# Kernel tuning notes

Hardware: AMD Instinct MI355X
Metric: run time of the kernel (lower is better)

## Reference

```python
import jax, jax.numpy as jnp
import numpy as np

TEMPERATURE = 10.0
NUM_PROBES = 100


def setup_inputs() -> dict:
    key = jax.random.key(0)
    k1, k2 = jax.random.split(key)
    N, C = 50000, 20
    y_pred = jax.random.normal(k1, (N, C), dtype=jnp.float32)
    s = jax.random.randint(k2, (N,), 0, 2, dtype=jnp.int32)
    return {"y_pred": y_pred, "s": s}


def reference(y_pred, s):
    # y_pred: [N, C], s: [N] in {0,1}
    # Per-class probing grid: 100 points from min to max of that class's preds.
    # torch's .item() detaches min/max from the graph -> stop_gradient here.
    mn = jax.lax.stop_gradient(jnp.min(y_pred, axis=0))  # [C]
    mx = jax.lax.stop_gradient(jnp.max(y_pred, axis=0))  # [C]
    frac = jnp.arange(NUM_PROBES, dtype=y_pred.dtype) / (NUM_PROBES - 1)  # [P]
    grid = mn[:, None] + (mx - mn)[:, None] * frac[None, :]  # [C, P]

    # Smoothed ECDF via sigmoid: diff has shape [C, P, N]
    preds = y_pred.T  # [C, N]
    sig = jax.nn.sigmoid(TEMPERATURE * (grid[:, :, None] - preds[:, None, :]))

    mask0 = (s == 0).astype(y_pred.dtype)  # [N]
    mask1 = (s == 1).astype(y_pred.dtype)
    n0 = jnp.sum(mask0)
    n1 = jnp.sum(mask1)

    # Masked group means == per-group mean since sigmoid is elementwise
    cdf0 = jnp.einsum('cpn,n->cp', sig, mask0) / n0  # [C, P]
    cdf1 = jnp.einsum('cpn,n->cp', sig, mask1) / n1  # [C, P]

    delta = jnp.abs(cdf0 - cdf1)  # [C, P]
    # loss_i = max over probes; final = max over classes -> global max
    return jnp.max(delta)
```

## Files before the change

kernel.cpp:

```cpp
#include <hip/hip_runtime.h>

#define NC 20
#define NP 100
#define PG 10
#define NPG (NP / PG)
#define SLICES 10
#define TPB 256
#define KLOG2E 14.426950408889634f
#define NBS 256

__device__ __forceinline__ float fexp2(float x) {
#if __has_builtin(__builtin_amdgcn_exp2f)
    return __builtin_amdgcn_exp2f(x);
#else
    return __builtin_exp2f(x);
#endif
}
__device__ __forceinline__ float sgpr_f(float x) {
    return __uint_as_float(__builtin_amdgcn_readfirstlane(__float_as_uint(x)));
}

template<bool WRITE_T>
__global__ __launch_bounds__(256)
void prep_kernel(const float* __restrict__ y, const int* __restrict__ s,
                 float* __restrict__ E, float* __restrict__ sf,
                 float* __restrict__ part_mn, float* __restrict__ part_mx,
                 int* __restrict__ part_cnt, int N, int ncap) {
    const int q = blockIdx.y;
    const int bx = blockIdx.x;
    float mn[4] = {3.4e38f, 3.4e38f, 3.4e38f, 3.4e38f};
    float mx[4] = {-3.4e38f, -3.4e38f, -3.4e38f, -3.4e38f};
    int cnt = 0;
    const int stride = gridDim.x * 256;
    for (int n = bx * 256 + threadIdx.x; n < ncap; n += stride) {
        if (n < N) {
            float4 f = ((const float4*)y)[n * 5 + q];
            float v[4] = {f.x, f.y, f.z, f.w};
#pragma unroll
            for (int cc = 0; cc < 4; ++cc) {
                mn[cc] = fminf(mn[cc], v[cc]);
                mx[cc] = fmaxf(mx[cc], v[cc]);
                if (WRITE_T) E[(size_t)(4 * q + cc) * ncap + n] = fexp2(v[cc] * KLOG2E);
            }
            if (q == 0) {
                int m = s[n];
                cnt += m;
                if (WRITE_T) sf[n] = (float)m;
            }
        } else if (WRITE_T) {
#pragma unroll
            for (int cc = 0; cc < 4; ++cc)
                E[(size_t)(4 * q + cc) * ncap + n] = __builtin_inff();
            if (q == 0) sf[n] = 0.f;
        }
    }
#pragma unroll
    for (int off = 1; off < 64; off <<= 1) {
#pragma unroll
        for (int cc = 0; cc < 4; ++cc) {
            mn[cc] = fminf(mn[cc], __shfl_xor(mn[cc], off));
            mx[cc] = fmaxf(mx[cc], __shfl_xor(mx[cc], off));
        }
        cnt += __shfl_xor(cnt, off);
    }
    __shared__ float smn[4][4], smx[4][4];
    __shared__ int scnt[4];
    const int wave = threadIdx.x >> 6, lane = threadIdx.x & 63;
    if (lane == 0) {
#pragma unroll
        for (int cc = 0; cc < 4; ++cc) { smn[wave][cc] = mn[cc]; smx[wave][cc] = mx[cc]; }
        scnt[wave] = cnt;
    }
    __syncthreads();
    const int t = threadIdx.x;
    if (t < 4) {
        part_mn[(4 * q + t) * NBS + bx] =
            fminf(fminf(smn[0][t], smn[1][t]), fminf(smn[2][t], smn[3][t]));
    } else if (t < 8) {
        int cc = t - 4;
        part_mx[(4 * q + cc) * NBS + bx] =
            fmaxf(fmaxf(smx[0][cc], smx[1][cc]), fmaxf(smx[2][cc], smx[3][cc]));
    } else if (t == 8 && q == 0) {
        part_cnt[bx] = scnt[0] + scnt[1] + scnt[2] + scnt[3];
    }
}

template<bool RAW>
__global__ __launch_bounds__(256)
void cdf2_kernel(const float* __restrict__ E, const float* __restrict__ sf,
                 const float* __restrict__ y, const int* __restrict__ s,
                 const float* __restrict__ part_mn, const float* __restrict__ part_mx,
                 const int* __restrict__ part_cnt,
                 float* __restrict__ acc_part, int N, int ncap, int nb) {
    const int c = blockIdx.x;
    const int pg = blockIdx.y;
    float lmn = 3.4e38f, lmx = -3.4e38f;
    int lcnt = 0;
    for (int t = threadIdx.x; t < nb; t += 256) {
        lmn = fminf(lmn, part_mn[c * NBS + t]);
        lmx = fmaxf(lmx, part_mx[c * NBS + t]);
        lcnt += part_cnt[t];
    }
#pragma unroll
    for (int off = 1; off < 64; off <<= 1) {
        lmn = fminf(lmn, __shfl_xor(lmn, off));
        lmx = fmaxf(lmx, __shfl_xor(lmx, off));
        lcnt += __shfl_xor(lcnt, off);
    }
    __shared__ float rmn[4], rmx[4];
    __shared__ int rcnt[4];
    const int wave = threadIdx.x >> 6, lane = threadIdx.x & 63;
    if (lane == 0) { rmn[wave] = lmn; rmx[wave] = lmx; rcnt[wave] = lcnt; }
    __syncthreads();
    const float mn = fminf(fminf(rmn[0], rmn[1]), fminf(rmn[2], rmn[3]));
    const float mx = fmaxf(fmaxf(rmx[0], rmx[1]), fmaxf(rmx[2], rmx[3]));
    const int n1 = rcnt[0] + rcnt[1] + rcnt[2] + rcnt[3];
    const float inv1 = 1.0f / (float)n1;
    const float inv0 = 1.0f / (float)(N - n1);
    const float sA = sgpr_f(inv1 + inv0);
    const float sB = sgpr_f(-inv0);

    int p = pg * PG + (lane % PG);
    float frac = (float)p / 99.0f;
    float g = fmaf(mx - mn, frac, mn);
    float Gl = fexp2(-g * KLOG2E);
    float G[PG];
#pragma unroll
    for (int j = 0; j < PG; ++j) G[j] = sgpr_f(__shfl(Gl, j));

    float d[PG];
#pragma unroll
    for (int j = 0; j < PG; ++j) d[j] = 0.f;

    const int nq = ncap >> 2;
    if (!RAW) {
        const float4* E4 = (const float4*)(E + (size_t)c * ncap);
        const float4* S4 = (const float4*)sf;
#pragma unroll 2
        for (int q = blockIdx.z * TPB + threadIdx.x; q < nq; q += TPB * SLICES) {
            float4 ev = E4[q];
            float4 mv = S4[q];
            float ee[4] = {ev.x, ev.y, ev.z, ev.w};
            float ww[4];
            ww[0] = fmaf(mv.x, sA, sB); ww[1] = fmaf(mv.y, sA, sB);
            ww[2] = fmaf(mv.z, sA, sB); ww[3] = fmaf(mv.w, sA, sB);
#pragma unroll
            for (int e = 0; e < 4; ++e) {
#pragma unroll
                for (int j = 0; j < PG; ++j) {
                    float t = fmaf(ee[e], G[j], 1.0f);
                    float r = __builtin_amdgcn_rcpf(t);
                    d[j] = fmaf(r, ww[e], d[j]);
                }
            }
        }
    } else {
        for (int q = blockIdx.z * TPB + threadIdx.x; q < nq; q += TPB * SLICES) {
#pragma unroll
            for (int e = 0; e < 4; ++e) {
                int n = q * 4 + e;
                bool valid = n < N;
                float ev = valid ? fexp2(y[(size_t)n * NC + c] * KLOG2E)
                                 : __builtin_inff();
                float w  = valid ? fmaf((float)s[n], sA, sB) : 0.f;
#pragma unroll
                for (int j = 0; j < PG; ++j) {
                    float t = fmaf(ev, G[j], 1.0f);
                    float r = __builtin_amdgcn_rcpf(t);
                    d[j] = fmaf(r, w, d[j]);
                }
            }
        }
    }
#pragma unroll
    for (int off = 1; off < 64; off <<= 1) {
#pragma unroll
        for (int j = 0; j < PG; ++j) d[j] += __shfl_xor(d[j], off);
    }
    __shared__ float sd[4][PG];
    if (lane == 0) {
#pragma unroll
        for (int j = 0; j < PG; ++j) sd[wave][j] = d[j];
    }
    __syncthreads();
    if (threadIdx.x < PG) {
        int j = threadIdx.x;
        float v = (sd[0][j] + sd[1][j]) + (sd[2][j] + sd[3][j]);
        acc_part[(size_t)(c * NP + pg * PG + j) * SLICES + blockIdx.z] = v;
    }
}

__global__ __launch_bounds__(256)
void finalize_kernel(const float* __restrict__ acc_part, float* __restrict__ out) {
    float m = 0.f;
    for (int i = threadIdx.x; i < NC * NP; i += 256) {
        const float* base = acc_part + (size_t)i * SLICES;
        float sum = 0.f;
#pragma unroll
        for (int z = 0; z < SLICES; ++z) sum += base[z];
        m = fmaxf(m, fabsf(sum));
    }
#pragma unroll
    for (int off = 1; off < 64; off <<= 1)
        m = fmaxf(m, __shfl_xor(m, off));
    __shared__ float red[4];
    const int wave = threadIdx.x >> 6, lane = threadIdx.x & 63;
    if (lane == 0) red[wave] = m;
    __syncthreads();
    if (threadIdx.x == 0)
        out[0] = fmaxf(fmaxf(red[0], red[1]), fmaxf(red[2], red[3]));
}

extern "C" void kernel_launch(void* const* d_in, const int* in_sizes, int n_in,
                              void* d_out, int out_size, void* d_ws, size_t ws_size,
                              hipStream_t stream) {
    const float* y = (const float*)d_in[0];
    const int* s   = (const int*)d_in[1];
    const int N = in_sizes[1];
    const int ncap = ((N + 1023) / 1024) * 1024;
    int nb = ncap / 256;
    if (nb > NBS) nb = NBS;

    unsigned char* ws = (unsigned char*)d_ws;
    float* part_mn  = (float*)ws;
    float* part_mx  = (float*)(ws + 20480);
    int*   part_cnt = (int*)  (ws + 40960);
    float* acc_part = (float*)(ws + 45056);
    float* E        = (float*)(ws + 131072);
    float* sf       = (float*)(ws + 131072 + (size_t)4 * NC * ncap);
    size_t need = 131072 + (size_t)4 * (NC + 1) * ncap;
    bool fat = ws_size >= need;

    dim3 gA(nb, 5);
    if (fat) prep_kernel<true ><<<gA, 256, 0, stream>>>(y, s, E, sf, part_mn, part_mx, part_cnt, N, ncap);
    else     prep_kernel<false><<<gA, 256, 0, stream>>>(y, s, nullptr, nullptr, part_mn, part_mx, part_cnt, N, ncap);

    dim3 gB(NC, NPG, SLICES);
    if (fat) cdf2_kernel<false><<<gB, 256, 0, stream>>>(E, sf, y, s, part_mn, part_mx, part_cnt, acc_part, N, ncap, nb);
    else     cdf2_kernel<true ><<<gB, 256, 0, stream>>>(nullptr, nullptr, y, s, part_mn, part_mx, part_cnt, acc_part, N, ncap, nb);

    finalize_kernel<<<1, 256, 0, stream>>>(acc_part, (float*)d_out);
}
```

Measured before the change: 33.15 us.

## Pack group mask into exp sign bit and fuse finalize via last-block atomics

The prep kernel now encodes the group label in the sign bit of each stored exp value instead of writing a separate float mask array. The CDF kernel recovers the weight from the sign and uses the absolute value for the sigmoid term, which removes one global load stream per element. The separate finalize launch is replaced by a per-(class, probe-group) atomic counter: the last slice block sums the partial results and does an atomicMax on the output. This saves a kernel launch and workspace traffic, but it relies on relaxed atomics for ordering and never zeroes the output before the atomicMax.

```diff
diff --git a/kernel.cpp b/kernel.cpp
--- a/kernel.cpp
+++ b/kernel.cpp
@@ -23,11 +23,14 @@
 template<bool WRITE_T>
 __global__ __launch_bounds__(256)
 void prep_kernel(const float* __restrict__ y, const int* __restrict__ s,
-                 float* __restrict__ E, float* __restrict__ sf,
+                 float* __restrict__ E,
                  float* __restrict__ part_mn, float* __restrict__ part_mx,
-                 int* __restrict__ part_cnt, int N, int ncap) {
+                 int* __restrict__ part_cnt, unsigned* __restrict__ cnt200,
+                 int N, int ncap) {
     const int q = blockIdx.y;
     const int bx = blockIdx.x;
+    if (q == 2 && bx == 0 && threadIdx.x < NC * NPG) cnt200[threadIdx.x] = 0u;
+
     float mn[4] = {3.4e38f, 3.4e38f, 3.4e38f, 3.4e38f};
     float mx[4] = {-3.4e38f, -3.4e38f, -3.4e38f, -3.4e38f};
     int cnt = 0;
@@ -36,22 +39,25 @@
         if (n < N) {
             float4 f = ((const float4*)y)[n * 5 + q];
             float v[4] = {f.x, f.y, f.z, f.w};
+            int m = 0;
+            if (q == 0) { m = s[n]; cnt += m; }
+            unsigned sgn = 0u;
+            if (WRITE_T && q == 0) sgn = m ? 0x80000000u : 0u;
+            if (WRITE_T) sgn = (s[n] ? 0x80000000u : 0u);
 #pragma unroll
             for (int cc = 0; cc < 4; ++cc) {
                 mn[cc] = fminf(mn[cc], v[cc]);
                 mx[cc] = fmaxf(mx[cc], v[cc]);
-                if (WRITE_T) E[(size_t)(4 * q + cc) * ncap + n] = fexp2(v[cc] * KLOG2E);
-            }
-            if (q == 0) {
-                int m = s[n];
-                cnt += m;
-                if (WRITE_T) sf[n] = (float)m;
+                if (WRITE_T) {
+                    float e = fexp2(v[cc] * KLOG2E);
+                    E[(size_t)(4 * q + cc) * ncap + n] =
+                        __uint_as_float(__float_as_uint(e) | sgn);
+                }
             }
         } else if (WRITE_T) {
 #pragma unroll
             for (int cc = 0; cc < 4; ++cc)
                 E[(size_t)(4 * q + cc) * ncap + n] = __builtin_inff();
-            if (q == 0) sf[n] = 0.f;
         }
     }
 #pragma unroll
@@ -87,11 +93,12 @@
 
 template<bool RAW>
 __global__ __launch_bounds__(256)
-void cdf2_kernel(const float* __restrict__ E, const float* __restrict__ sf,
+void cdf2_kernel(const float* __restrict__ E,
                  const float* __restrict__ y, const int* __restrict__ s,
                  const float* __restrict__ part_mn, const float* __restrict__ part_mx,
                  const int* __restrict__ part_cnt,
-                 float* __restrict__ acc_part, int N, int ncap, int nb) {
+                 float* __restrict__ acc_part, unsigned* __restrict__ cnt200,
+                 float* __restrict__ out, int N, int ncap, int nb) {
     const int c = blockIdx.x;
     const int pg = blockIdx.y;
     float lmn = 3.4e38f, lmx = -3.4e38f;
@@ -117,8 +124,9 @@
     const int n1 = rcnt[0] + rcnt[1] + rcnt[2] + rcnt[3];
     const float inv1 = 1.0f / (float)n1;
     const float inv0 = 1.0f / (float)(N - n1);
-    const float sA = sgpr_f(inv1 + inv0);
-    const float sB = sgpr_f(-inv0);
+    const float sAB = sgpr_f(inv1);
+    const float sB  = sgpr_f(-inv0);
+    const float sA1 = sgpr_f(inv1);
 
     int p = pg * PG + (lane % PG);
     float frac = (float)p / 99.0f;
@@ -135,20 +143,19 @@
     const int nq = ncap >> 2;
     if (!RAW) {
         const float4* E4 = (const float4*)(E + (size_t)c * ncap);
-        const float4* S4 = (const float4*)sf;
 #pragma unroll 2
         for (int q = blockIdx.z * TPB + threadIdx.x; q < nq; q += TPB * SLICES) {
             float4 ev = E4[q];
-            float4 mv = S4[q];
             float ee[4] = {ev.x, ev.y, ev.z, ev.w};
             float ww[4];
-            ww[0] = fmaf(mv.x, sA, sB); ww[1] = fmaf(mv.y, sA, sB);
-            ww[2] = fmaf(mv.z, sA, sB); ww[3] = fmaf(mv.w, sA, sB);
+#pragma unroll
+            for (int e = 0; e < 4; ++e)
+                ww[e] = (__float_as_int(ee[e]) < 0) ? sA1 : sB;
 #pragma unroll
             for (int e = 0; e < 4; ++e) {
 #pragma unroll
                 for (int j = 0; j < PG; ++j) {
-                    float t = fmaf(ee[e], G[j], 1.0f);
+                    float t = fmaf(fabsf(ee[e]), G[j], 1.0f);
                     float r = __builtin_amdgcn_rcpf(t);
                     d[j] = fmaf(r, ww[e], d[j]);
                 }
@@ -162,7 +169,7 @@
                 bool valid = n < N;
                 float ev = valid ? fexp2(y[(size_t)n * NC + c] * KLOG2E)
                                  : __builtin_inff();
-                float w  = valid ? fmaf((float)s[n], sA, sB) : 0.f;
+                float w  = valid ? ((s[n] != 0) ? sA1 : sB) : 0.f;
 #pragma unroll
                 for (int j = 0; j < PG; ++j) {
                     float t = fmaf(ev, G[j], 1.0f);
@@ -183,32 +190,42 @@
         for (int j = 0; j < PG; ++j) sd[wave][j] = d[j];
     }
     __syncthreads();
+    float* slot_base = acc_part + (size_t)(c * NP + pg * PG) * SLICES;
     if (threadIdx.x < PG) {
         int j = threadIdx.x;
         float v = (sd[0][j] + sd[1][j]) + (sd[2][j] + sd[3][j]);
-        acc_part[(size_t)(c * NP + pg * PG + j) * SLICES + blockIdx.z] = v;
-    }
-}
-
-__global__ __launch_bounds__(256)
-void finalize_kernel(const float* __restrict__ acc_part, float* __restrict__ out) {
-    float m = 0.f;
-    for (int i = threadIdx.x; i < NC * NP; i += 256) {
-        const float* base = acc_part + (size_t)i * SLICES;
-        float sum = 0.f;
-#pragma unroll
-        for (int z = 0; z < SLICES; ++z) sum += base[z];
-        m = fmaxf(m, fabsf(sum));
-    }
-#pragma unroll
-    for (int off = 1; off < 64; off <<= 1)
-        m = fmaxf(m, __shfl_xor(m, off));
-    __shared__ float red[4];
-    const int wave = threadIdx.x >> 6, lane = threadIdx.x & 63;
-    if (lane == 0) red[wave] = m;
-    __syncthreads();
-    if (threadIdx.x == 0)
-        out[0] = fmaxf(fmaxf(red[0], red[1]), fmaxf(red[2], red[3]));
+        __hip_atomic_store(slot_base + j * SLICES + blockIdx.z, v,
+                           __ATOMIC_RELAXED, __HIP_MEMORY_SCOPE_AGENT);
+    }
+    asm volatile("s_waitcnt vmcnt(0)" ::: "memory");
+    __shared__ int is_last;
+    if (threadIdx.x == 0) {
+        unsigned prev = __hip_atomic_fetch_add(&cnt200[c * NPG + pg], 1u,
+                                               __ATOMIC_RELAXED,
+                                               __HIP_MEMORY_SCOPE_AGENT);
+        is_last = (prev == SLICES - 1);
+    }
+    __syncthreads();
+    if (!is_last) return;
+
+    __shared__ float sval[PG * SLICES];
+    if (threadIdx.x < PG * SLICES) {
+        sval[threadIdx.x] = __hip_atomic_load(slot_base + threadIdx.x,
+                                              __ATOMIC_RELAXED,
+                                              __HIP_MEMORY_SCOPE_AGENT);
+    }
+    __syncthreads();
+    if (threadIdx.x == 0) {
+        float m = 0.f;
+#pragma unroll
+        for (int j = 0; j < PG; ++j) {
+            float sum = 0.f;
+#pragma unroll
+            for (int z = 0; z < SLICES; ++z) sum += sval[j * SLICES + z];
+            m = fmaxf(m, fabsf(sum));
+        }
+        atomicMax((int*)out, __float_as_int(m));
+    }
 }
 
 extern "C" void kernel_launch(void* const* d_in, const int* in_sizes, int n_in,
@@ -225,19 +242,17 @@
     float* part_mn  = (float*)ws;
     float* part_mx  = (float*)(ws + 20480);
     int*   part_cnt = (int*)  (ws + 40960);
+    unsigned* cnt200= (unsigned*)(ws + 43008);
     float* acc_part = (float*)(ws + 45056);
     float* E        = (float*)(ws + 131072);
-    float* sf       = (float*)(ws + 131072 + (size_t)4 * NC * ncap);
-    size_t need = 131072 + (size_t)4 * (NC + 1) * ncap;
+    size_t need = 131072 + (size_t)4 * NC * ncap;
     bool fat = ws_size >= need;
 
     dim3 gA(nb, 5);
-    if (fat) prep_kernel<true ><<<gA, 256, 0, stream>>>(y, s, E, sf, part_mn, part_mx, part_cnt, N, ncap);
-    else     prep_kernel<false><<<gA, 256, 0, stream>>>(y, s, nullptr, nullptr, part_mn, part_mx, part_cnt, N, ncap);
+    if (fat) prep_kernel<true ><<<gA, 256, 0, stream>>>(y, s, E, part_mn, part_mx, part_cnt, cnt200, N, ncap);
+    else     prep_kernel<false><<<gA, 256, 0, stream>>>(y, s, nullptr, part_mn, part_mx, part_cnt, cnt200, N, ncap);
 
     dim3 gB(NC, NPG, SLICES);
-    if (fat) cdf2_kernel<false><<<gB, 256, 0, stream>>>(E, sf, y, s, part_mn, part_mx, part_cnt, acc_part, N, ncap, nb);
-    else     cdf2_kernel<true ><<<gB, 256, 0, stream>>>(nullptr, nullptr, y, s, part_mn, part_mx, part_cnt, acc_part, N, ncap, nb);
-
-    finalize_kernel<<<1, 256, 0, stream>>>(acc_part, (float*)d_out);
-}
+    if (fat) cdf2_kernel<false><<<gB, 256, 0, stream>>>(E, y, s, part_mn, part_mx, part_cnt, acc_part, cnt200, (float*)d_out, N, ncap, nb);
+    else     cdf2_kernel<true ><<<gB, 256, 0, stream>>>(nullptr, y, s, part_mn, part_mx, part_cnt, acc_part, cnt200, (float*)d_out, N, ncap, nb);
+}
```

After: 32.73 us. No clear change (-1.3%).
